# Kernel tuning notes

Measured on AMD Instinct MI355X. Metric: run time of the kernel, lower is better.

Reference implementation:

```python
import jax, jax.numpy as jnp
import numpy as np

UNITS = 512


def setup_inputs() -> dict:
    key = jax.random.key(0)
    ks = jax.random.split(key, 9)
    B, D, U = 16384, 512, UNITS
    return {
        "inputs": jax.random.normal(ks[0], (B, 2 * D), dtype=jnp.float32),
        "h": jax.random.normal(ks[1], (B, U), dtype=jnp.float32),
        "w_z": jax.random.normal(ks[2], (D, U), dtype=jnp.float32) * 0.05,
        "u_z": jax.random.normal(ks[3], (U, U), dtype=jnp.float32) * 0.05,
        "b_z": jnp.zeros((U,), dtype=jnp.float32),
        "w_r": jax.random.normal(ks[4], (D, U), dtype=jnp.float32) * 0.05,
        "u_r": jax.random.normal(ks[5], (U, U), dtype=jnp.float32) * 0.05,
        "b_r": jnp.zeros((U,), dtype=jnp.float32),
        "w_h": jax.random.normal(ks[6], (D, U), dtype=jnp.float32) * 0.05,
        "u_h": jax.random.normal(ks[7], (U, U), dtype=jnp.float32) * 0.05,
        "b_h": jnp.zeros((U,), dtype=jnp.float32),
    }


def reference(inputs, h, w_z, u_z, b_z, w_r, u_r, b_r, w_h, u_h, b_h):
    # Split concatenated (input, mask) halves along the feature axis.
    x, mask = jnp.split(inputs, 2, axis=1)  # each (B, D)
    # Faithful to source: mask @ zeros((D, U)) is identically zero.
    out_mask = jnp.matmul(mask, jnp.zeros((mask.shape[-1], UNITS), dtype=inputs.dtype))  # (B, U)
    h_masked = h * out_mask
    z_t = jax.nn.sigmoid(jnp.matmul(x, w_z) + jnp.matmul(h_masked, u_z) + b_z)
    r_t = jax.nn.sigmoid(jnp.matmul(x, w_r) + jnp.matmul(h_masked, u_r) + b_r)
    h_t = jnp.tanh(jnp.matmul(x, w_h) + jnp.matmul(r_t * h_masked, u_h) + b_h)
    h_t_seq = z_t * h_t + (1.0 - z_t) * h_masked  # (B, U)
    h_t_forward = jnp.concatenate((h_t_seq, out_mask), axis=1)  # (B, 2U)
    return (h_t_forward, h_t_seq)
```

## Files before the change

kernel.cpp:

```cpp
#include <hip/hip_runtime.h>
#include <hip/hip_bf16.h>

typedef __attribute__((ext_vector_type(4))) float f32x4;
typedef __attribute__((ext_vector_type(8))) short short8;
typedef __attribute__((ext_vector_type(8))) unsigned short ushort8;
typedef __attribute__((ext_vector_type(4))) unsigned short ushort4v;

#define M_ROWS 16384
#define KDIM 512
#define UDIM 512
#define IN_STRIDE 1024
#define NSTEP 16

__device__ __forceinline__ unsigned short f2bf(float f) {
    union { float f; unsigned u; } v; v.f = f;
    unsigned r = v.u + 0x7FFFu + ((v.u >> 16) & 1u);
    return (unsigned short)(r >> 16);
}

__device__ __forceinline__ unsigned cvt2(float a, float b) {
    __hip_bfloat162 h = __float22bfloat162_rn(float2{a, b});
    union { __hip_bfloat162 h; unsigned u; } c; c.h = h; return c.u;
}

#define GLD16(g, l)                                                            \
    __builtin_amdgcn_global_load_lds(                                          \
        (const __attribute__((address_space(1))) void*)(g),                    \
        (__attribute__((address_space(3))) void*)(l), 16, 0, 0)

__global__ __launch_bounds__(256) void pack_w(
    const float* __restrict__ w_z,
    const float* __restrict__ w_h,
    unsigned short* __restrict__ Wp)
{
    int tid = blockIdx.x * 256 + threadIdx.x;
    int s   = tid & 511;
    int kt  = (tid >> 9) & 15;
    int ub  = tid >> 13;
    int jj  = s >> 2;
    int sl  = (s & 3) ^ ((jj >> 1) & 3);
    int k   = kt * 32 + sl * 8;
    const float* w = ((jj >> 5) & 1) ? w_h : w_z;
    int u = ub * 64 + ((jj >> 6) << 5) + (jj & 31);
    ushort8 v;
#pragma unroll
    for (int i = 0; i < 8; ++i)
        v[i] = f2bf(w[(size_t)(k + i) * UDIM + u]);
    *reinterpret_cast<ushort8*>(Wp + (size_t)tid * 8) = v;
}

__global__ __launch_bounds__(256, 4) void gru_gemm(
    const float* __restrict__ x,
    const unsigned short* __restrict__ Wp,
    const float* __restrict__ b_z,
    const float* __restrict__ b_h,
    float* __restrict__ out)
{
    __shared__ __align__(16) unsigned char smem[40960];
    unsigned short* shA = (unsigned short*)smem;
    unsigned short* shB = (unsigned short*)(smem + 16384);

    const int tid  = threadIdx.x;
    const int lane = tid & 63;
    const int wid  = tid >> 6;
    const int wm   = wid >> 1;
    const int wn   = wid & 1;

    const int d  = blockIdx.x;
    const int bx = (d >> 3) & 7;
    const int by = (d & 7) * 16 + (d >> 6);
    const int u0   = bx * 64;
    const int brow = by * 128;

    const int s0a = wid * 128 + lane;
    const int s1a = s0a + 64;
    const int r0 = s0a >> 2, r1 = s1a >> 2;
    const int q0 = (s0a & 3) ^ ((r0 >> 1) & 3);
    const int q1 = (s1a & 3) ^ ((r1 >> 1) & 3);
    const float* gA0 = x + (size_t)(brow + r0) * IN_STRIDE + q0 * 8;
    const float* gA1 = x + (size_t)(brow + r1) * IN_STRIDE + q1 * 8;

    const unsigned short* bp = Wp + (size_t)bx * 65536 + (size_t)s0a * 8;

    f32x4 acc[4][4];
#pragma unroll
    for (int m = 0; m < 4; ++m)
#pragma unroll
        for (int n = 0; n < 4; ++n)
            acc[m][n] = (f32x4){0.f, 0.f, 0.f, 0.f};

    f32x4 rA[2][4];

#define ISSUE_AREG(t, set)                                                     \
    {                                                                          \
        rA[set][0] = *reinterpret_cast<const f32x4*>(gA0 + (t) * 32);          \
        rA[set][1] = *reinterpret_cast<const f32x4*>(gA0 + (t) * 32 + 4);      \
        rA[set][2] = *reinterpret_cast<const f32x4*>(gA1 + (t) * 32);          \
        rA[set][3] = *reinterpret_cast<const f32x4*>(gA1 + (t) * 32 + 4);      \
    }

#define ISSUE_B(t, b)                                                          \
    {                                                                          \
        GLD16(bp + (size_t)(t) * 4096,       shB + (b) * 4096 + wid * 1024);   \
        GLD16(bp + (size_t)(t) * 4096 + 512, shB + (b) * 4096 + wid * 1024 + 512); \
    }

#define CVT_WRITE_A(set, b)                                                    \
    {                                                                          \
        union { unsigned u[4]; ushort8 v; } c0, c1;                            \
        c0.u[0] = cvt2(rA[set][0][0], rA[set][0][1]);                          \
        c0.u[1] = cvt2(rA[set][0][2], rA[set][0][3]);                          \
        c0.u[2] = cvt2(rA[set][1][0], rA[set][1][1]);                          \
        c0.u[3] = cvt2(rA[set][1][2], rA[set][1][3]);                          \
        c1.u[0] = cvt2(rA[set][2][0], rA[set][2][1]);                          \
        c1.u[1] = cvt2(rA[set][2][2], rA[set][2][3]);                          \
        c1.u[2] = cvt2(rA[set][3][0], rA[set][3][1]);                          \
        c1.u[3] = cvt2(rA[set][3][2], rA[set][3][3]);                          \
        *reinterpret_cast<ushort8*>(&shA[(b) * 4096 + s0a * 8]) = c0.v;        \
        *reinterpret_cast<ushort8*>(&shA[(b) * 4096 + s1a * 8]) = c1.v;        \
    }

    const int fr = lane & 15;
    const int ks = lane >> 4;
    const int xo = (fr >> 1) & 3;
    int aoff[4], boff[4];
#pragma unroll
    for (int m = 0; m < 4; ++m)
        aoff[m] = (wm * 64 + m * 16 + fr) * 32 + ((ks ^ xo) << 3);
#pragma unroll
    for (int n = 0; n < 4; ++n)
        boff[n] = (wn * 64 + n * 16 + fr) * 32 + ((ks ^ xo) << 3);

    ISSUE_AREG(0, 0); ISSUE_B(0, 0);
    ISSUE_AREG(1, 1); ISSUE_B(1, 1);
    asm volatile("s_waitcnt vmcnt(6)" ::: "memory");
    CVT_WRITE_A(0, 0);
    asm volatile("s_waitcnt lgkmcnt(0)" ::: "memory");
    asm volatile("s_barrier" ::: "memory");

#pragma unroll
    for (int t = 0; t < NSTEP; ++t) {
        if (t + 2 < NSTEP) {
            ISSUE_AREG(t + 2, t & 1);
            ISSUE_B(t + 2, (t + 2) % 3);
        }
        const int ba = t & 1, bb = t % 3;
        short8 af[4], bfrag[4];
#pragma unroll
        for (int m = 0; m < 4; ++m)
            af[m] = *reinterpret_cast<const short8*>(&shA[ba * 4096 + aoff[m]]);
#pragma unroll
        for (int n = 0; n < 4; ++n)
            bfrag[n] = *reinterpret_cast<const short8*>(&shB[bb * 4096 + boff[n]]);
#pragma unroll
        for (int m = 0; m < 4; ++m)
#pragma unroll
            for (int n = 0; n < 4; ++n)
                acc[m][n] = __builtin_amdgcn_mfma_f32_16x16x32_bf16(af[m], bfrag[n], acc[m][n], 0, 0, 0);
        if (t + 1 < NSTEP) {
            if (t + 2 < NSTEP) {
                asm volatile("s_waitcnt vmcnt(6)" ::: "memory");
            } else {
                asm volatile("s_waitcnt vmcnt(0)" ::: "memory");
            }
            CVT_WRITE_A((t + 1) & 1, (t + 1) & 1);
            asm volatile("s_waitcnt lgkmcnt(0)" ::: "memory");
            asm volatile("s_barrier" ::: "memory");
        }
    }

    __syncthreads();

    float* plane = (float*)smem;
    const int fq = lane >> 4;
#pragma unroll
    for (int p = 0; p < 2; ++p) {
        int ucol = wn * 32 + p * 16 + fr;
        float bz = b_z[u0 + ucol];
        float bh = b_h[u0 + ucol];
#pragma unroll
        for (int m = 0; m < 4; ++m) {
            int row0 = wm * 64 + m * 16 + fq * 4;
            f32x4 az = acc[m][p];
            f32x4 ah = acc[m][p + 2];
#pragma unroll
            for (int j = 0; j < 4; ++j) {
                float zt = 1.f / (1.f + __expf(-(az[j] + bz)));
                float e  = __expf(2.f * (ah[j] + bh));
                float s  = zt * (1.f - 2.f / (e + 1.f));
                plane[(row0 + j) * 68 + ucol] = s;
            }
        }
    }
    __syncthreads();

    float* fwd = out;
    float* seq = out + (size_t)M_ROWS * 1024;
    const f32x4 z4 = (f32x4){0.f, 0.f, 0.f, 0.f};
    const int c4 = (tid & 15) * 4;
#pragma unroll
    for (int it = 0; it < 8; ++it) {
        int row = it * 16 + (tid >> 4);
        f32x4 v = *reinterpret_cast<const f32x4*>(&plane[row * 68 + c4]);
        size_t grow = (size_t)(brow + row);
        *reinterpret_cast<f32x4*>(&fwd[grow * 1024 + u0 + c4])       = v;
        *reinterpret_cast<f32x4*>(&fwd[grow * 1024 + 512 + u0 + c4]) = z4;
        *reinterpret_cast<f32x4*>(&seq[grow * 512 + u0 + c4])        = v;
    }
#undef ISSUE_AREG
#undef ISSUE_B
#undef CVT_WRITE_A
}

#define LDSS 40
__global__ __launch_bounds__(256) void gru_fused_legacy(
    const float* __restrict__ inp, const float* __restrict__ w_z,
    const float* __restrict__ b_z, const float* __restrict__ w_h,
    const float* __restrict__ b_h, float* __restrict__ out)
{
    __shared__ __align__(16) unsigned short Asl[2][128][LDSS];
    __shared__ __align__(16) unsigned short Bsl[2][128][LDSS];
    const int tid = threadIdx.x, lane = tid & 63, wid = tid >> 6;
    const int wm = wid >> 1, wn = wid & 1;
    const int u0 = blockIdx.x * 64, brow = blockIdx.y * 128;
    f32x4 acc[4][4];
#pragma unroll
    for (int m = 0; m < 4; ++m)
#pragma unroll
        for (int n = 0; n < 4; ++n) acc[m][n] = (f32x4){0.f,0.f,0.f,0.f};
    f32x4 rA[4], rB[4];
#define STAGE_LOAD(kt) { const int k0_=(kt)*32; \
    _Pragma("unroll") for (int it=0; it<4; ++it){ int idx=tid+256*it; int r=idx>>3,c=(idx&7)<<2; \
        rA[it]=*reinterpret_cast<const f32x4*>(inp+(size_t)(brow+r)*IN_STRIDE+k0_+c);} \
    _Pragma("unroll") for (int it=0; it<4; ++it){ int idx=tid+256*it; int jj=idx&127; int k4=(idx>>7)<<2; \
        const float* w_=((jj>>5)&1)?w_h:w_z; int u_=u0+((jj>>6)<<5)+(jj&31); \
        const float* p_=w_+(size_t)(k0_+k4)*UDIM+u_; \
        rB[it][0]=p_[0]; rB[it][1]=p_[UDIM]; rB[it][2]=p_[2*UDIM]; rB[it][3]=p_[3*UDIM];} }
#define STAGE_WRITE(bufi) { \
    _Pragma("unroll") for (int it=0; it<4; ++it){ int idx=tid+256*it; int r=idx>>3,c=(idx&7)<<2; ushort4v v; \
        v[0]=f2bf(rA[it][0]); v[1]=f2bf(rA[it][1]); v[2]=f2bf(rA[it][2]); v[3]=f2bf(rA[it][3]); \
        *reinterpret_cast<ushort4v*>(&Asl[bufi][r][c])=v;} \
    _Pragma("unroll") for (int it=0; it<4; ++it){ int idx=tid+256*it; int jj=idx&127; int k4=(idx>>7)<<2; ushort4v v; \
        v[0]=f2bf(rB[it][0]); v[1]=f2bf(rB[it][1]); v[2]=f2bf(rB[it][2]); v[3]=f2bf(rB[it][3]); \
        *reinterpret_cast<ushort4v*>(&Bsl[bufi][jj][k4])=v;} }
    STAGE_LOAD(0); STAGE_WRITE(0);
    const int fr = lane & 15, koff = (lane >> 4) << 3;
    for (int kt = 0; kt < 16; ++kt) {
        if (kt + 1 < 16) STAGE_LOAD(kt + 1);
        __syncthreads();
        const int buf = kt & 1;
        short8 af[4], bfr[4];
#pragma unroll
        for (int m = 0; m < 4; ++m) af[m] = *reinterpret_cast<const short8*>(&Asl[buf][wm*64+m*16+fr][koff]);
#pragma unroll
        for (int n = 0; n < 4; ++n) bfr[n] = *reinterpret_cast<const short8*>(&Bsl[buf][wn*64+n*16+fr][koff]);
#pragma unroll
        for (int m = 0; m < 4; ++m)
#pragma unroll
            for (int n = 0; n < 4; ++n)
                acc[m][n] = __builtin_amdgcn_mfma_f32_16x16x32_bf16(af[m], bfr[n], acc[m][n], 0, 0, 0);
        if (kt + 1 < 16) STAGE_WRITE((kt + 1) & 1);
    }
    float* fwd = out; float* seq = out + (size_t)M_ROWS * 1024;
    const int fq = lane >> 4;
#pragma unroll
    for (int p = 0; p < 2; ++p) {
        int u = u0 + wn * 32 + p * 16 + fr;
        float bz = b_z[u], bh = b_h[u];
#pragma unroll
        for (int m = 0; m < 4; ++m) {
            int row0 = brow + wm * 64 + m * 16 + fq * 4;
            f32x4 az = acc[m][p], ah = acc[m][p + 2];
#pragma unroll
            for (int j = 0; j < 4; ++j) {
                float zt = 1.f / (1.f + __expf(-(az[j] + bz)));
                float e  = __expf(2.f * (ah[j] + bh));
                float s  = zt * (1.f - 2.f / (e + 1.f));
                size_t rr = (size_t)(row0 + j);
                fwd[rr * 1024 + u] = s;
                fwd[rr * 1024 + 512 + u] = 0.f;
                seq[rr * 512 + u] = s;
            }
        }
    }
}

extern "C" void kernel_launch(void* const* d_in, const int* in_sizes, int n_in,
                              void* d_out, int out_size, void* d_ws, size_t ws_size,
                              hipStream_t stream) {
    const float* inp = (const float*)d_in[0];
    const float* w_z = (const float*)d_in[2];
    const float* b_z = (const float*)d_in[4];
    const float* w_h = (const float*)d_in[8];
    const float* b_h = (const float*)d_in[10];
    float* out = (float*)d_out;

    const size_t needW = (size_t)8 * 16 * 512 * 16;
    if (ws_size >= needW) {
        unsigned short* Wp = (unsigned short*)d_ws;
        hipLaunchKernelGGL(pack_w, dim3(256), dim3(256), 0, stream, w_z, w_h, Wp);
        hipLaunchKernelGGL(gru_gemm, dim3(1024), dim3(256), 0, stream,
                           inp, Wp, b_z, b_h, out);
    } else {
        hipLaunchKernelGGL(gru_fused_legacy, dim3(8, 128), dim3(256), 0, stream,
                           inp, w_z, b_z, w_h, b_h, out);
    }
}
```

Before: 46.14 us.

## Deepen A-operand register prefetch to three stages and move conversion before MFMA

Triple-buffers the fp32 A-tile register loads, so global loads are issued three steps ahead instead of two. The bf16 conversion and LDS write for the next step now sit between the fragment reads and the MFMA block, letting them overlap with matrix math. The main loop is hand-unrolled with per-step vmcnt wait values. Occupancy hint drops from 4 to 3 waves per SIMD to make room for the extra registers, which may reduce latency hiding across waves.

```diff
diff --git a/kernel.cpp b/kernel.cpp
--- a/kernel.cpp
+++ b/kernel.cpp
@@ -49,7 +49,7 @@
     *reinterpret_cast<ushort8*>(Wp + (size_t)tid * 8) = v;
 }
 
-__global__ __launch_bounds__(256, 4) void gru_gemm(
+__global__ __launch_bounds__(256, 3) void gru_gemm(
     const float* __restrict__ x,
     const unsigned short* __restrict__ Wp,
     const float* __restrict__ b_z,
@@ -89,15 +89,18 @@
         for (int n = 0; n < 4; ++n)
             acc[m][n] = (f32x4){0.f, 0.f, 0.f, 0.f};
 
-    f32x4 rA[2][4];
-
-#define ISSUE_AREG(t, set)                                                     \
+    f32x4 a0_0, a0_1, a0_2, a0_3;
+    f32x4 a1_0, a1_1, a1_2, a1_3;
+    f32x4 a2_0, a2_1, a2_2, a2_3;
+
+#define ISSUE_A_(t, s)                                                         \
     {                                                                          \
-        rA[set][0] = *reinterpret_cast<const f32x4*>(gA0 + (t) * 32);          \
-        rA[set][1] = *reinterpret_cast<const f32x4*>(gA0 + (t) * 32 + 4);      \
-        rA[set][2] = *reinterpret_cast<const f32x4*>(gA1 + (t) * 32);          \
-        rA[set][3] = *reinterpret_cast<const f32x4*>(gA1 + (t) * 32 + 4);      \
-    }
+        a##s##_0 = *reinterpret_cast<const f32x4*>(gA0 + (t) * 32);            \
+        a##s##_1 = *reinterpret_cast<const f32x4*>(gA0 + (t) * 32 + 4);        \
+        a##s##_2 = *reinterpret_cast<const f32x4*>(gA1 + (t) * 32);            \
+        a##s##_3 = *reinterpret_cast<const f32x4*>(gA1 + (t) * 32 + 4);        \
+    }
+#define ISSUE_A(t, s) ISSUE_A_(t, s)
 
 #define ISSUE_B(t, b)                                                          \
     {                                                                          \
@@ -105,20 +108,24 @@
         GLD16(bp + (size_t)(t) * 4096 + 512, shB + (b) * 4096 + wid * 1024 + 512); \
     }
 
-#define CVT_WRITE_A(set, b)                                                    \
+#define CVT_WRITE_A_(s, b)                                                     \
     {                                                                          \
         union { unsigned u[4]; ushort8 v; } c0, c1;                            \
-        c0.u[0] = cvt2(rA[set][0][0], rA[set][0][1]);                          \
-        c0.u[1] = cvt2(rA[set][0][2], rA[set][0][3]);                          \
-        c0.u[2] = cvt2(rA[set][1][0], rA[set][1][1]);                          \
-        c0.u[3] = cvt2(rA[set][1][2], rA[set][1][3]);                          \
-        c1.u[0] = cvt2(rA[set][2][0], rA[set][2][1]);                          \
-        c1.u[1] = cvt2(rA[set][2][2], rA[set][2][3]);                          \
-        c1.u[2] = cvt2(rA[set][3][0], rA[set][3][1]);                          \
-        c1.u[3] = cvt2(rA[set][3][2], rA[set][3][3]);                          \
+        c0.u[0] = cvt2(a##s##_0[0], a##s##_0[1]);                              \
+        c0.u[1] = cvt2(a##s##_0[2], a##s##_0[3]);                              \
+        c0.u[2] = cvt2(a##s##_1[0], a##s##_1[1]);                              \
+        c0.u[3] = cvt2(a##s##_1[2], a##s##_1[3]);                              \
+        c1.u[0] = cvt2(a##s##_2[0], a##s##_2[1]);                              \
+        c1.u[1] = cvt2(a##s##_2[2], a##s##_2[3]);                              \
+        c1.u[2] = cvt2(a##s##_3[0], a##s##_3[1]);                              \
+        c1.u[3] = cvt2(a##s##_3[2], a##s##_3[3]);                              \
         *reinterpret_cast<ushort8*>(&shA[(b) * 4096 + s0a * 8]) = c0.v;        \
         *reinterpret_cast<ushort8*>(&shA[(b) * 4096 + s1a * 8]) = c1.v;        \
     }
+#define CVT_WRITE_A(s, b) CVT_WRITE_A_(s, b)
+
+#define VMWAIT_(n) asm volatile("s_waitcnt vmcnt(" #n ")" ::: "memory")
+#define VMWAIT(n) VMWAIT_(n)
 
     const int fr = lane & 15;
     const int ks = lane >> 4;
@@ -131,43 +138,47 @@
     for (int n = 0; n < 4; ++n)
         boff[n] = (wn * 64 + n * 16 + fr) * 32 + ((ks ^ xo) << 3);
 
-    ISSUE_AREG(0, 0); ISSUE_B(0, 0);
-    ISSUE_AREG(1, 1); ISSUE_B(1, 1);
-    asm volatile("s_waitcnt vmcnt(6)" ::: "memory");
+    ISSUE_A(0, 0);
+    ISSUE_B(0, 0);
+    ISSUE_A(1, 1);
+    ISSUE_B(1, 1);
+    ISSUE_A(2, 2);
+    VMWAIT(10);
     CVT_WRITE_A(0, 0);
     asm volatile("s_waitcnt lgkmcnt(0)" ::: "memory");
     asm volatile("s_barrier" ::: "memory");
 
-#pragma unroll
-    for (int t = 0; t < NSTEP; ++t) {
-        if (t + 2 < NSTEP) {
-            ISSUE_AREG(t + 2, t & 1);
-            ISSUE_B(t + 2, (t + 2) % 3);
-        }
-        const int ba = t & 1, bb = t % 3;
-        short8 af[4], bfrag[4];
-#pragma unroll
-        for (int m = 0; m < 4; ++m)
-            af[m] = *reinterpret_cast<const short8*>(&shA[ba * 4096 + aoff[m]]);
-#pragma unroll
-        for (int n = 0; n < 4; ++n)
-            bfrag[n] = *reinterpret_cast<const short8*>(&shB[bb * 4096 + boff[n]]);
-#pragma unroll
-        for (int m = 0; m < 4; ++m)
-#pragma unroll
-            for (int n = 0; n < 4; ++n)
-                acc[m][n] = __builtin_amdgcn_mfma_f32_16x16x32_bf16(af[m], bfrag[n], acc[m][n], 0, 0, 0);
-        if (t + 1 < NSTEP) {
-            if (t + 2 < NSTEP) {
-                asm volatile("s_waitcnt vmcnt(6)" ::: "memory");
-            } else {
-                asm volatile("s_waitcnt vmcnt(0)" ::: "memory");
-            }
-            CVT_WRITE_A((t + 1) & 1, (t + 1) & 1);
-            asm volatile("s_waitcnt lgkmcnt(0)" ::: "memory");
-            asm volatile("s_barrier" ::: "memory");
-        }
-    }
+#define STEP(T, SW, SI, VM)                                                    \
+    {                                                                          \
+        if ((T) + 2 < NSTEP) ISSUE_B((T) + 2, ((T) + 2) % 3);                  \
+        short8 af[4], bfrag[4];                                                \
+        _Pragma("unroll")                                                      \
+        for (int m = 0; m < 4; ++m)                                            \
+            af[m] = *reinterpret_cast<const short8*>(                          \
+                &shA[((T) & 1) * 4096 + aoff[m]]);                             \
+        _Pragma("unroll")                                                      \
+        for (int n = 0; n < 4; ++n)                                            \
+            bfrag[n] = *reinterpret_cast<const short8*>(                       \
+                &shB[((T) % 3) * 4096 + boff[n]]);                             \
+        if ((T) + 1 < NSTEP) CVT_WRITE_A(SW, ((T) + 1) & 1);                   \
+        if ((T) + 3 < NSTEP) ISSUE_A((T) + 3, SI);                             \
+        _Pragma("unroll")                                                      \
+        for (int m = 0; m < 4; ++m)                                            \
+            _Pragma("unroll")                                                  \
+            for (int n = 0; n < 4; ++n)                                        \
+                acc[m][n] = __builtin_amdgcn_mfma_f32_16x16x32_bf16(           \
+                    af[m], bfrag[n], acc[m][n], 0, 0, 0);                      \
+        if ((T) + 1 < NSTEP) {                                                 \
+            VMWAIT(VM);                                                        \
+            asm volatile("s_waitcnt lgkmcnt(0)" ::: "memory");                 \
+            asm volatile("s_barrier" ::: "memory");                            \
+        }                                                                      \
+    }
+
+    STEP(0, 1, 0, 6)   STEP(1, 2, 1, 6)   STEP(2, 0, 2, 6)   STEP(3, 1, 0, 6)
+    STEP(4, 2, 1, 6)   STEP(5, 0, 2, 6)   STEP(6, 1, 0, 6)   STEP(7, 2, 1, 6)
+    STEP(8, 0, 2, 6)   STEP(9, 1, 0, 6)   STEP(10, 2, 1, 6)  STEP(11, 0, 2, 6)
+    STEP(12, 1, 0, 6)  STEP(13, 2, 1, 2)  STEP(14, 0, 2, 0)  STEP(15, 1, 0, 0)
 
     __syncthreads();
 
@@ -207,9 +218,14 @@
         *reinterpret_cast<f32x4*>(&fwd[grow * 1024 + 512 + u0 + c4]) = z4;
         *reinterpret_cast<f32x4*>(&seq[grow * 512 + u0 + c4])        = v;
     }
-#undef ISSUE_AREG
+#undef STEP
+#undef ISSUE_A
+#undef ISSUE_A_
 #undef ISSUE_B
 #undef CVT_WRITE_A
+#undef CVT_WRITE_A_
+#undef VMWAIT
+#undef VMWAIT_
 }
 
 #define LDSS 40
```

New measurement: 49.76 us. 1.08x slower.

## Enlarge GEMM tile to 128x256 with 8 waves, K-step 64 and phased MFMA

Applied to the files above, without the earlier changes.

The GEMM block now has 512 threads (8 waves) and covers 128 rows by 128 output units, with both z and h gates, giving an effective N of 256. Each K-step is 64 wide using double-buffered LDS, 96KB in total. The weight pack layout and swizzle change to match. The MFMA loop is split into four phases that interleave the next tile's global loads and use setprio around MFMA bursts. This targets halving x re-reads across the N tiles and raising arithmetic intensity per LDS byte. The cost is lower occupancy from large LDS use and extra barriers per phase.

```diff
diff --git a/kernel.cpp b/kernel.cpp
--- a/kernel.cpp
+++ b/kernel.cpp
@@ -10,7 +10,7 @@
 #define KDIM 512
 #define UDIM 512
 #define IN_STRIDE 1024
-#define NSTEP 16
+#define NKT 8
 
 __device__ __forceinline__ unsigned short f2bf(float f) {
     union { float f; unsigned u; } v; v.f = f;
@@ -33,54 +33,57 @@
     const float* __restrict__ w_h,
     unsigned short* __restrict__ Wp)
 {
-    int tid = blockIdx.x * 256 + threadIdx.x;
-    int s   = tid & 511;
-    int kt  = (tid >> 9) & 15;
-    int ub  = tid >> 13;
-    int jj  = s >> 2;
-    int sl  = (s & 3) ^ ((jj >> 1) & 3);
-    int k   = kt * 32 + sl * 8;
-    const float* w = ((jj >> 5) & 1) ? w_h : w_z;
-    int u = ub * 64 + ((jj >> 6) << 5) + (jj & 31);
+    int g  = blockIdx.x * 256 + threadIdx.x;
+    int s  = g & 2047;
+    int kt = (g >> 11) & 7;
+    int bx = g >> 14;
+    int r  = s >> 3;
+    int p  = s & 7;
+    int l  = p ^ (r & 7);
+    int k0 = kt * 64 + l * 8;
+    int wn   = r >> 6;
+    int gate = (r >> 5) & 1;
+    int u    = bx * 128 + wn * 32 + (r & 31);
+    const float* w = gate ? w_h : w_z;
     ushort8 v;
 #pragma unroll
     for (int i = 0; i < 8; ++i)
-        v[i] = f2bf(w[(size_t)(k + i) * UDIM + u]);
-    *reinterpret_cast<ushort8*>(Wp + (size_t)tid * 8) = v;
-}
-
-__global__ __launch_bounds__(256, 4) void gru_gemm(
+        v[i] = f2bf(w[(size_t)(k0 + i) * UDIM + u]);
+    *reinterpret_cast<ushort8*>(Wp + (size_t)g * 8) = v;
+}
+
+__global__ __launch_bounds__(512, 2) void gru_gemm(
     const float* __restrict__ x,
     const unsigned short* __restrict__ Wp,
     const float* __restrict__ b_z,
     const float* __restrict__ b_h,
     float* __restrict__ out)
 {
-    __shared__ __align__(16) unsigned char smem[40960];
+    __shared__ __align__(16) unsigned char smem[98304];
     unsigned short* shA = (unsigned short*)smem;
-    unsigned short* shB = (unsigned short*)(smem + 16384);
+    unsigned short* shB = (unsigned short*)(smem + 32768);
 
     const int tid  = threadIdx.x;
     const int lane = tid & 63;
     const int wid  = tid >> 6;
-    const int wm   = wid >> 1;
-    const int wn   = wid & 1;
+    const int wm   = wid >> 2;
+    const int wn   = wid & 3;
 
     const int d  = blockIdx.x;
-    const int bx = (d >> 3) & 7;
-    const int by = (d & 7) * 16 + (d >> 6);
-    const int u0   = bx * 64;
+    const int t  = (d >> 3) + (d & 7) * 64;
+    const int by = t >> 2;
+    const int bx = t & 3;
     const int brow = by * 128;
-
-    const int s0a = wid * 128 + lane;
-    const int s1a = s0a + 64;
-    const int r0 = s0a >> 2, r1 = s1a >> 2;
-    const int q0 = (s0a & 3) ^ ((r0 >> 1) & 3);
-    const int q1 = (s1a & 3) ^ ((r1 >> 1) & 3);
-    const float* gA0 = x + (size_t)(brow + r0) * IN_STRIDE + q0 * 8;
-    const float* gA1 = x + (size_t)(brow + r1) * IN_STRIDE + q1 * 8;
-
-    const unsigned short* bp = Wp + (size_t)bx * 65536 + (size_t)s0a * 8;
+    const int u0t  = bx * 128;
+
+    const int sA0 = tid, sA1 = tid + 512;
+    const int rA0 = sA0 >> 3, rA1 = sA1 >> 3;
+    const int lA0 = (sA0 & 7) ^ (rA0 & 7);
+    const int lA1 = (sA1 & 7) ^ (rA1 & 7);
+    const float* gxA0 = x + (size_t)(brow + rA0) * IN_STRIDE + lA0 * 8;
+    const float* gxA1 = x + (size_t)(brow + rA1) * IN_STRIDE + lA1 * 8;
+
+    const unsigned short* bp = Wp + (size_t)bx * 8 * 2048 * 8;
 
     f32x4 acc[4][4];
 #pragma unroll
@@ -89,82 +92,96 @@
         for (int n = 0; n < 4; ++n)
             acc[m][n] = (f32x4){0.f, 0.f, 0.f, 0.f};
 
-    f32x4 rA[2][4];
-
-#define ISSUE_AREG(t, set)                                                     \
+    f32x4 as0lo, as0hi, as1lo, as1hi;
+
+#define ISSUE_A(kt1)                                                           \
     {                                                                          \
-        rA[set][0] = *reinterpret_cast<const f32x4*>(gA0 + (t) * 32);          \
-        rA[set][1] = *reinterpret_cast<const f32x4*>(gA0 + (t) * 32 + 4);      \
-        rA[set][2] = *reinterpret_cast<const f32x4*>(gA1 + (t) * 32);          \
-        rA[set][3] = *reinterpret_cast<const f32x4*>(gA1 + (t) * 32 + 4);      \
-    }
-
-#define ISSUE_B(t, b)                                                          \
+        as0lo = *reinterpret_cast<const f32x4*>(gxA0 + (kt1) * 64);            \
+        as0hi = *reinterpret_cast<const f32x4*>(gxA0 + (kt1) * 64 + 4);        \
+        as1lo = *reinterpret_cast<const f32x4*>(gxA1 + (kt1) * 64);            \
+        as1hi = *reinterpret_cast<const f32x4*>(gxA1 + (kt1) * 64 + 4);        \
+    }
+
+#define ISSUE_B2(kt1, q0_)                                                     \
     {                                                                          \
-        GLD16(bp + (size_t)(t) * 4096,       shB + (b) * 4096 + wid * 1024);   \
-        GLD16(bp + (size_t)(t) * 4096 + 512, shB + (b) * 4096 + wid * 1024 + 512); \
-    }
-
-#define CVT_WRITE_A(set, b)                                                    \
+        GLD16(bp + ((size_t)(kt1) * 2048 + tid + (q0_) * 512) * 8,             \
+              shB + ((kt1) & 1) * 16384 + (tid + (q0_) * 512) * 8);            \
+        GLD16(bp + ((size_t)(kt1) * 2048 + tid + ((q0_) + 1) * 512) * 8,       \
+              shB + ((kt1) & 1) * 16384 + (tid + ((q0_) + 1) * 512) * 8);      \
+    }
+
+#define CVT_WRITE_A(kt1)                                                       \
     {                                                                          \
         union { unsigned u[4]; ushort8 v; } c0, c1;                            \
-        c0.u[0] = cvt2(rA[set][0][0], rA[set][0][1]);                          \
-        c0.u[1] = cvt2(rA[set][0][2], rA[set][0][3]);                          \
-        c0.u[2] = cvt2(rA[set][1][0], rA[set][1][1]);                          \
-        c0.u[3] = cvt2(rA[set][1][2], rA[set][1][3]);                          \
-        c1.u[0] = cvt2(rA[set][2][0], rA[set][2][1]);                          \
-        c1.u[1] = cvt2(rA[set][2][2], rA[set][2][3]);                          \
-        c1.u[2] = cvt2(rA[set][3][0], rA[set][3][1]);                          \
-        c1.u[3] = cvt2(rA[set][3][2], rA[set][3][3]);                          \
-        *reinterpret_cast<ushort8*>(&shA[(b) * 4096 + s0a * 8]) = c0.v;        \
-        *reinterpret_cast<ushort8*>(&shA[(b) * 4096 + s1a * 8]) = c1.v;        \
+        c0.u[0] = cvt2(as0lo[0], as0lo[1]); c0.u[1] = cvt2(as0lo[2], as0lo[3]);\
+        c0.u[2] = cvt2(as0hi[0], as0hi[1]); c0.u[3] = cvt2(as0hi[2], as0hi[3]);\
+        c1.u[0] = cvt2(as1lo[0], as1lo[1]); c1.u[1] = cvt2(as1lo[2], as1lo[3]);\
+        c1.u[2] = cvt2(as1hi[0], as1hi[1]); c1.u[3] = cvt2(as1hi[2], as1hi[3]);\
+        *reinterpret_cast<ushort8*>(&shA[((kt1) & 1) * 8192 + sA0 * 8]) = c0.v;\
+        *reinterpret_cast<ushort8*>(&shA[((kt1) & 1) * 8192 + sA1 * 8]) = c1.v;\
     }
 
     const int fr = lane & 15;
     const int ks = lane >> 4;
-    const int xo = (fr >> 1) & 3;
-    int aoff[4], boff[4];
-#pragma unroll
-    for (int m = 0; m < 4; ++m)
-        aoff[m] = (wm * 64 + m * 16 + fr) * 32 + ((ks ^ xo) << 3);
-#pragma unroll
-    for (int n = 0; n < 4; ++n)
-        boff[n] = (wn * 64 + n * 16 + fr) * 32 + ((ks ^ xo) << 3);
-
-    ISSUE_AREG(0, 0); ISSUE_B(0, 0);
-    ISSUE_AREG(1, 1); ISSUE_B(1, 1);
-    asm volatile("s_waitcnt vmcnt(6)" ::: "memory");
-    CVT_WRITE_A(0, 0);
+    int aoffs[4][2], boffs[4][2];
+#pragma unroll
+    for (int i = 0; i < 4; ++i)
+#pragma unroll
+        for (int s32 = 0; s32 < 2; ++s32) {
+            int ra = wm * 64 + i * 16 + fr;
+            aoffs[i][s32] = (ra * 8 + ((s32 * 4 + ks) ^ (ra & 7))) * 8;
+            int rb = wn * 64 + i * 16 + fr;
+            boffs[i][s32] = (rb * 8 + ((s32 * 4 + ks) ^ (rb & 7))) * 8;
+        }
+
+    ISSUE_A(0);
+    ISSUE_B2(0, 0);
+    ISSUE_B2(0, 2);
+    asm volatile("s_waitcnt vmcnt(0)" ::: "memory");
+    CVT_WRITE_A(0);
     asm volatile("s_waitcnt lgkmcnt(0)" ::: "memory");
     asm volatile("s_barrier" ::: "memory");
 
 #pragma unroll
-    for (int t = 0; t < NSTEP; ++t) {
-        if (t + 2 < NSTEP) {
-            ISSUE_AREG(t + 2, t & 1);
-            ISSUE_B(t + 2, (t + 2) % 3);
-        }
-        const int ba = t & 1, bb = t % 3;
-        short8 af[4], bfrag[4];
-#pragma unroll
-        for (int m = 0; m < 4; ++m)
-            af[m] = *reinterpret_cast<const short8*>(&shA[ba * 4096 + aoff[m]]);
-#pragma unroll
-        for (int n = 0; n < 4; ++n)
-            bfrag[n] = *reinterpret_cast<const short8*>(&shB[bb * 4096 + boff[n]]);
-#pragma unroll
-        for (int m = 0; m < 4; ++m)
-#pragma unroll
-            for (int n = 0; n < 4; ++n)
-                acc[m][n] = __builtin_amdgcn_mfma_f32_16x16x32_bf16(af[m], bfrag[n], acc[m][n], 0, 0, 0);
-        if (t + 1 < NSTEP) {
-            if (t + 2 < NSTEP) {
-                asm volatile("s_waitcnt vmcnt(6)" ::: "memory");
-            } else {
+    for (int kt = 0; kt < NKT; ++kt) {
+        const int abase = (kt & 1) * 8192;
+        const int bbase = (kt & 1) * 16384;
+#pragma unroll
+        for (int ph = 0; ph < 4; ++ph) {
+            const int mh = ph >> 1, nh = ph & 1;
+            short8 af[2][2], bf[2][2];
+#pragma unroll
+            for (int i2 = 0; i2 < 2; ++i2)
+#pragma unroll
+                for (int s32 = 0; s32 < 2; ++s32) {
+                    af[i2][s32] = *reinterpret_cast<const short8*>(
+                        &shA[abase + aoffs[mh * 2 + i2][s32]]);
+                    bf[i2][s32] = *reinterpret_cast<const short8*>(
+                        &shB[bbase + boffs[nh * 2 + i2][s32]]);
+                }
+            if (kt + 1 < NKT) {
+                if (ph == 0) { ISSUE_A(kt + 1); ISSUE_B2(kt + 1, 0); }
+                if (ph == 1) { ISSUE_B2(kt + 1, 2); }
+            }
+            asm volatile("s_barrier" ::: "memory");
+            asm volatile("s_waitcnt lgkmcnt(0)" ::: "memory");
+            __builtin_amdgcn_s_setprio(1);
+#pragma unroll
+            for (int i2 = 0; i2 < 2; ++i2)
+#pragma unroll
+                for (int j2 = 0; j2 < 2; ++j2)
+#pragma unroll
+                    for (int s32 = 0; s32 < 2; ++s32)
+                        acc[mh * 2 + i2][nh * 2 + j2] =
+                            __builtin_amdgcn_mfma_f32_16x16x32_bf16(
+                                af[i2][s32], bf[j2][s32],
+                                acc[mh * 2 + i2][nh * 2 + j2], 0, 0, 0);
+            __builtin_amdgcn_s_setprio(0);
+            if (ph == 3 && kt + 1 < NKT) {
                 asm volatile("s_waitcnt vmcnt(0)" ::: "memory");
+                CVT_WRITE_A(kt + 1);
+                asm volatile("s_waitcnt lgkmcnt(0)" ::: "memory");
             }
-            CVT_WRITE_A((t + 1) & 1, (t + 1) & 1);
-            asm volatile("s_waitcnt lgkmcnt(0)" ::: "memory");
             asm volatile("s_barrier" ::: "memory");
         }
     }
@@ -172,23 +189,23 @@
     __syncthreads();
 
     float* plane = (float*)smem;
-    const int fq = lane >> 4;
+    const int fq = ks;
 #pragma unroll
     for (int p = 0; p < 2; ++p) {
         int ucol = wn * 32 + p * 16 + fr;
-        float bz = b_z[u0 + ucol];
-        float bh = b_h[u0 + ucol];
-#pragma unroll
-        for (int m = 0; m < 4; ++m) {
-            int row0 = wm * 64 + m * 16 + fq * 4;
-            f32x4 az = acc[m][p];
-            f32x4 ah = acc[m][p + 2];
+        float bz = b_z[u0t + ucol];
+        float bh = b_h[u0t + ucol];
+#pragma unroll
+        for (int mi = 0; mi < 4; ++mi) {
+            int row0 = wm * 64 + mi * 16 + fq * 4;
+            f32x4 az = acc[mi][p];
+            f32x4 ah = acc[mi][p + 2];
 #pragma unroll
             for (int j = 0; j < 4; ++j) {
                 float zt = 1.f / (1.f + __expf(-(az[j] + bz)));
                 float e  = __expf(2.f * (ah[j] + bh));
                 float s  = zt * (1.f - 2.f / (e + 1.f));
-                plane[(row0 + j) * 68 + ucol] = s;
+                plane[(row0 + j) * 132 + ucol] = s;
             }
         }
     }
@@ -197,18 +214,19 @@
     float* fwd = out;
     float* seq = out + (size_t)M_ROWS * 1024;
     const f32x4 z4 = (f32x4){0.f, 0.f, 0.f, 0.f};
-    const int c4 = (tid & 15) * 4;
 #pragma unroll
     for (int it = 0; it < 8; ++it) {
-        int row = it * 16 + (tid >> 4);
-        f32x4 v = *reinterpret_cast<const f32x4*>(&plane[row * 68 + c4]);
+        int idx = it * 512 + tid;
+        int row = idx >> 5;
+        int c4  = (idx & 31) * 4;
+        f32x4 v = *reinterpret_cast<const f32x4*>(&plane[row * 132 + c4]);
         size_t grow = (size_t)(brow + row);
-        *reinterpret_cast<f32x4*>(&fwd[grow * 1024 + u0 + c4])       = v;
-        *reinterpret_cast<f32x4*>(&fwd[grow * 1024 + 512 + u0 + c4]) = z4;
-        *reinterpret_cast<f32x4*>(&seq[grow * 512 + u0 + c4])        = v;
-    }
-#undef ISSUE_AREG
-#undef ISSUE_B
+        *reinterpret_cast<f32x4*>(&fwd[grow * 1024 + u0t + c4])       = v;
+        *reinterpret_cast<f32x4*>(&fwd[grow * 1024 + 512 + u0t + c4]) = z4;
+        *reinterpret_cast<f32x4*>(&seq[grow * 512 + u0t + c4])        = v;
+    }
+#undef ISSUE_A
+#undef ISSUE_B2
 #undef CVT_WRITE_A
 }
 
@@ -295,11 +313,11 @@
     const float* b_h = (const float*)d_in[10];
     float* out = (float*)d_out;
 
-    const size_t needW = (size_t)8 * 16 * 512 * 16;
+    const size_t needW = (size_t)4 * 8 * 2048 * 16;
     if (ws_size >= needW) {
         unsigned short* Wp = (unsigned short*)d_ws;
         hipLaunchKernelGGL(pack_w, dim3(256), dim3(256), 0, stream, w_z, w_h, Wp);
-        hipLaunchKernelGGL(gru_gemm, dim3(1024), dim3(256), 0, stream,
+        hipLaunchKernelGGL(gru_gemm, dim3(512), dim3(512), 0, stream,
                            inp, Wp, b_z, b_h, out);
     } else {
         hipLaunchKernelGGL(gru_fused_legacy, dim3(8, 128), dim3(256), 0, stream,
```

After: 54.56 us. 1.18x slower.
